# Kernel optimization log

Hardware: AMD Instinct MI355X
Metric: run time of the kernel (lower is better)

## Reference

```python
import jax, jax.numpy as jnp
import numpy as np

N = 100000   # nodes in batched graph
E = 1600000  # edges
B = 2048     # number of user/item pairs (target links)
IN = 4       # one-hot node label dim
H = 32       # latent dim per layer
R = 5        # num relations (rating levels)
NB = 2       # num bases
L = 4        # num conv layers


def setup_inputs() -> dict:
    key = jax.random.key(0)
    ks = jax.random.split(key, 16)
    s = 0.1
    # node labels: first B nodes are users (class 0), next B items (class 1), rest hop labels {2,3}
    cls = jax.random.randint(ks[0], (N,), 2, IN)
    cls = cls.at[:B].set(0).at[B:2 * B].set(1)
    x = jax.nn.one_hot(cls, IN, dtype=jnp.float32)
    src = jax.random.randint(ks[1], (E,), 0, N)
    dst = jax.random.randint(ks[2], (E,), 0, N)
    etype = jax.random.randint(ks[3], (E,), 0, R)
    V0 = jax.random.normal(ks[4], (NB, IN, H), jnp.float32) * s
    comp0 = jax.random.normal(ks[5], (R, NB), jnp.float32) * s
    loop0 = jax.random.normal(ks[6], (IN, H), jnp.float32) * s
    bias0 = jnp.zeros((H,), jnp.float32)
    Vs = jax.random.normal(ks[7], (L - 1, NB, H, H), jnp.float32) * s
    comps = jax.random.normal(ks[8], (L - 1, R, NB), jnp.float32) * s
    loops = jax.random.normal(ks[9], (L - 1, H, H), jnp.float32) * s
    biases = jnp.zeros((L - 1, H), jnp.float32)
    w1 = jax.random.normal(ks[10], (128, 2 * L * H), jnp.float32) * 0.05
    b1 = jnp.zeros((128,), jnp.float32)
    w2 = jax.random.normal(ks[11], (1, 128), jnp.float32) * 0.05
    b2 = jnp.zeros((1,), jnp.float32)
    return {"x": x, "src": src, "dst": dst, "etype": etype,
            "V0": V0, "comp0": comp0, "loop0": loop0, "bias0": bias0,
            "Vs": Vs, "comps": comps, "loops": loops, "biases": biases,
            "w1": w1, "b1": b1, "w2": w2, "b2": b2}


def _rgcn(h, src, dst, etype, V, comp, loopW, bias):
    # basis-decomposed RelGraphConv: W_r = sum_b comp[r,b] * V[b]
    # precompute per-basis transforms at nodes, then combine per edge by relation coeff
    xb = jnp.einsum('ni,bio->nbo', h, V)            # [N, NB, out]
    m = jnp.einsum('eb,ebo->eo', comp[etype], xb[src])  # [E, out]
    agg = jax.ops.segment_sum(m, dst, num_segments=h.shape[0])  # sum aggregation
    return agg + h @ loopW + bias                   # self-loop + bias


def reference(x, src, dst, etype, V0, comp0, loop0, bias0, Vs, comps, loops, biases, w1, b1, w2, b2):
    states = []
    h = jnp.tanh(_rgcn(x, src, dst, etype, V0, comp0, loop0, bias0))
    states.append(h)
    for i in range(L - 1):
        h = jnp.tanh(_rgcn(h, src, dst, etype, Vs[i], comps[i], loops[i], biases[i]))
        states.append(h)
    cs = jnp.concatenate(states, axis=1)            # [N, L*H]
    # users are nodes [0,B), items are nodes [B,2B) by construction (x[:,0]==1 / x[:,1]==1)
    feat = jnp.concatenate([cs[:B], cs[B:2 * B]], axis=1)  # [B, 2*L*H]
    hid = jax.nn.relu(feat @ w1.T + b1)             # dropout inactive (eval)
    out = (hid @ w2.T + b2)[:, 0] * 1               # multiply_by = 1
    return out
```

## Files before the change

### kernel.cpp

```cpp
#include <hip/hip_runtime.h>
#include <hip/hip_fp16.h>

constexpr int N_  = 100000;
constexpr int E_  = 1600000;
constexpr int B_  = 2048;
constexpr int NT_ = 2 * B_;

constexpr int NPB_SHIFT = 9;
constexpr int NPB = 1 << NPB_SHIFT;
constexpr int KB_ = (N_ + NPB - 1) / NPB;
constexpr int CAP_ = 9216;
constexpr int PCHUNK = 8192;
constexpr int NPBLK = (E_ + PCHUNK - 1) / PCHUNK;

__global__ __launch_bounds__(256) void init_kernel(
    const float* __restrict__ x, const float* __restrict__ w1,
    unsigned char* __restrict__ cls, int* __restrict__ flag,
    int* __restrict__ cnt, int* __restrict__ bcur, float* __restrict__ w1t)
{
    const int b = blockIdx.x, t = threadIdx.x;
    if (b < 391) {
        const int n = b * 256 + t;
        if (n < N_) {
            const float4 v = *(const float4*)(x + n * 4);
            cls[n] = v.y > 0.5f ? 1 : (v.z > 0.5f ? 2 : (v.w > 0.5f ? 3 : 0));
            flag[n] = 0;
        }
        if (b == 0 && t == 0) *cnt = 0;
    } else if (b < 519) {
        const int idx = (b - 391) * 256 + t;
        const int j = idx >> 8, k = idx & 255;
        w1t[k * 128 + j] = w1[idx];
    } else {
        if (t < KB_) bcur[t] = 0;
    }
}

__global__ __launch_bounds__(256) void partition_kernel(
    const int* __restrict__ src, const int* __restrict__ dst,
    const int* __restrict__ etype, int* __restrict__ bcur, int* __restrict__ ebuf)
{
    __shared__ int hist[KB_];
    __shared__ int gbase[KB_];
    __shared__ int lcur[KB_];
    const int t = threadIdx.x;
    for (int i = t; i < KB_; i += 256) { hist[i] = 0; lcur[i] = 0; }
    __syncthreads();
    const int e0 = blockIdx.x * PCHUNK;
    const int e1 = min(e0 + PCHUNK, E_);
    for (int i = e0 + t; i < e1; i += 256) atomicAdd(&hist[dst[i] >> NPB_SHIFT], 1);
    __syncthreads();
    for (int i = t; i < KB_; i += 256) if (hist[i]) gbase[i] = atomicAdd(&bcur[i], hist[i]);
    __syncthreads();
    for (int i = e0 + t; i < e1; i += 256) {
        const int d = dst[i];
        const int b = d >> NPB_SHIFT;
        const int lp = atomicAdd(&lcur[b], 1);
        ebuf[(size_t)b * CAP_ + gbase[b] + lp] = src[i] | (etype[i] << 17) | ((d & (NPB - 1)) << 20);
    }
}

__global__ __launch_bounds__(256) void bscan_kernel(
    const int* __restrict__ bcur, int* __restrict__ boffs)
{
    __shared__ int sh[256];
    const int t = threadIdx.x;
    const int v = (t < KB_) ? bcur[t] : 0;
    sh[t] = v; __syncthreads();
#pragma unroll
    for (int off = 1; off < 256; off <<= 1) {
        const int u = (t >= off) ? sh[t - off] : 0;
        __syncthreads();
        sh[t] += u;
        __syncthreads();
    }
    if (t < KB_) boffs[t] = sh[t] - v;
    if (t == 0) boffs[KB_] = E_;
}

__global__ __launch_bounds__(512) void bfinish_kernel(
    const int* __restrict__ bcur, const int* __restrict__ boffs,
    const int* __restrict__ ebuf, const unsigned char* __restrict__ cls,
    const float* __restrict__ comp0, const float* __restrict__ V0,
    const float* __restrict__ loop0, const float* __restrict__ bias0,
    int* __restrict__ rowptr, int* __restrict__ pack,
    float* __restrict__ cs, __half* __restrict__ hout)
{
    __shared__ int cnt[NPB];
    __shared__ int sh[NPB];
    __shared__ unsigned int hist[NPB * 20];
    __shared__ float sLoop[128], sV0[256], sBias[32], sCmp[10];
    const int b = blockIdx.x, t = threadIdx.x;
    const int s0 = b * CAP_;
    const int s1 = s0 + bcur[b];
    const int db = boffs[b];
    cnt[t] = 0;
    for (int i = t; i < NPB * 20; i += 512) hist[i] = 0u;
    if (t < 128) sLoop[t] = loop0[t];
    if (t < 256) sV0[t]   = V0[t];
    if (t < 32)  sBias[t] = bias0[t];
    if (t < 10)  sCmp[t]  = comp0[t];
    __syncthreads();
    for (int i = s0 + t; i < s1; i += 512) {
        const int p = ebuf[i];
        const int dloc = p >> 20;
        const int et = (p >> 17) & 7;
        const int c = cls[p & 0x1FFFF];
        atomicAdd(&cnt[dloc], 1);
        atomicAdd(&hist[dloc * 20 + et * 4 + c], 1u);
    }
    __syncthreads();
    const int v = cnt[t];
    sh[t] = v; __syncthreads();
#pragma unroll
    for (int off = 1; off < NPB; off <<= 1) {
        const int u = (t >= off) ? sh[t - off] : 0;
        __syncthreads();
        sh[t] += u;
        __syncthreads();
    }
    const int rp = db + sh[t] - v;
    const int node = (b << NPB_SHIFT) + t;
    if (node < N_) rowptr[node] = rp;
    cnt[t] = rp;
    if (b == 0 && t == 0) rowptr[N_] = E_;
    __syncthreads();
    for (int i = s0 + t; i < s1; i += 512) {
        const int p = ebuf[i];
        const int pos = atomicAdd(&cnt[p >> 20], 1);
        pack[pos] = p & 0xFFFFF;
    }
    if (node < N_) {
        float A0[4], A1[4];
#pragma unroll
        for (int j = 0; j < 4; ++j) {
            float a0 = 0.f, a1 = 0.f;
#pragma unroll
            for (int r = 0; r < 5; ++r) {
                const float c = (float)hist[t * 20 + r * 4 + j];
                a0 += c * sCmp[r * 2];
                a1 += c * sCmp[r * 2 + 1];
            }
            A0[j] = a0; A1[j] = a1;
        }
        const int myc = cls[node];
        __half hrow[32];
        const bool wcs = node < NT_;
#pragma unroll 8
        for (int d = 0; d < 32; ++d) {
            float o = sBias[d] + sLoop[myc * 32 + d];
#pragma unroll
            for (int j = 0; j < 4; ++j)
                o += A0[j] * sV0[j * 32 + d] + A1[j] * sV0[128 + j * 32 + d];
            const float r = tanhf(o);
            hrow[d] = __float2half(r);
            if (wcs) cs[node * 128 + d] = r;
        }
        uint4* dst4 = (uint4*)(hout + (size_t)node * 32);
        const uint4* src4 = (const uint4*)hrow;
        dst4[0] = src4[0]; dst4[1] = src4[1]; dst4[2] = src4[2]; dst4[3] = src4[3];
    }
}

__global__ __launch_bounds__(256) void flagcompact_kernel(
    const int* __restrict__ rowptr, const int* __restrict__ pack,
    int* __restrict__ flag, int* __restrict__ cnt, int* __restrict__ nlist)
{
    const int lim = rowptr[NT_];
    const int tid = blockIdx.x * 256 + threadIdx.x;
    if (tid < NT_) nlist[atomicAdd(cnt, 1)] = tid;
    const int stride = gridDim.x * 256;
    for (int i = tid; i < lim; i += stride) {
        const int s = pack[i] & 0x1FFFF;
        if (s >= NT_ && atomicExch(&flag[s], 1) == 0)
            nlist[atomicAdd(cnt, 1)] = s;
    }
}

__device__ __forceinline__ void acc_chunk(
    const uint4& v, int pq, bool ok, const float* cmp, float* a0, float* a1)
{
    const int tt = (pq >> 17) & 7;
    const float c0 = ok ? cmp[tt * 2]     : 0.f;
    const float c1 = ok ? cmp[tt * 2 + 1] : 0.f;
    const __half2* hp = (const __half2*)&v;
#pragma unroll
    for (int k = 0; k < 4; ++k) {
        const float2 f = __half22float2(hp[k]);
        a0[2 * k]     += c0 * f.x;
        a0[2 * k + 1] += c0 * f.y;
        a1[2 * k]     += c1 * f.x;
        a1[2 * k + 1] += c1 * f.y;
    }
}

__device__ __forceinline__ float gather_body(
    int n, int lane, int g,
    const __half* __restrict__ hin, const int* __restrict__ rowptr,
    const int* __restrict__ pack, const float* cmp,
    const float* __restrict__ V, const float* __restrict__ loopW,
    const float* __restrict__ bias, float (*hs)[96])
{
    hs[g][lane] = __half2float(hin[n * 32 + lane]);
    const int beg = rowptr[n], end = rowptr[n + 1];
    const int sg = lane >> 2;
    const int c  = lane & 31 & 3;
    const int i0 = beg + sg, i1 = i0 + 8, i2 = i0 + 16, i3 = i0 + 24;
    const int p0 = pack[i0 < end ? i0 : beg];
    const int p1 = pack[i1 < end ? i1 : beg];
    const int p2 = pack[i2 < end ? i2 : beg];
    const int p3 = pack[i3 < end ? i3 : beg];
    const uint4 v0 = *(const uint4*)(hin + (size_t)(p0 & 0x1FFFF) * 32 + c * 8);
    const uint4 v1 = *(const uint4*)(hin + (size_t)(p1 & 0x1FFFF) * 32 + c * 8);
    const uint4 v2 = *(const uint4*)(hin + (size_t)(p2 & 0x1FFFF) * 32 + c * 8);
    const uint4 v3 = *(const uint4*)(hin + (size_t)(p3 & 0x1FFFF) * 32 + c * 8);
    float a0[8] = {0.f,0.f,0.f,0.f,0.f,0.f,0.f,0.f};
    float a1[8] = {0.f,0.f,0.f,0.f,0.f,0.f,0.f,0.f};
    acc_chunk(v0, p0, i0 < end, cmp, a0, a1);
    acc_chunk(v1, p1, i1 < end, cmp, a0, a1);
    acc_chunk(v2, p2, i2 < end, cmp, a0, a1);
    acc_chunk(v3, p3, i3 < end, cmp, a0, a1);
    for (int e0 = beg + 32; e0 < end; e0 += 8) {
        const int e = e0 + sg;
        const bool ok = e < end;
        const int p = pack[ok ? e : beg];
        const uint4 u = *(const uint4*)(hin + (size_t)(p & 0x1FFFF) * 32 + c * 8);
        acc_chunk(u, p, ok, cmp, a0, a1);
    }
#pragma unroll
    for (int k = 0; k < 8; ++k) {
        a0[k] += __shfl_xor(a0[k], 4);
        a0[k] += __shfl_xor(a0[k], 8);
        a0[k] += __shfl_xor(a0[k], 16);
        a1[k] += __shfl_xor(a1[k], 4);
        a1[k] += __shfl_xor(a1[k], 8);
        a1[k] += __shfl_xor(a1[k], 16);
    }
    if (lane < 4) {
#pragma unroll
        for (int k = 0; k < 8; ++k) {
            hs[g][32 + c * 8 + k] = a0[k];
            hs[g][64 + c * 8 + k] = a1[k];
        }
    }
    __builtin_amdgcn_wave_barrier();
    float o = bias[lane];
#pragma unroll 8
    for (int k = 0; k < 32; ++k) {
        o += hs[g][k] * loopW[k * 32 + lane]
           + hs[g][32 + k] * V[k * 32 + lane]
           + hs[g][64 + k] * V[1024 + k * 32 + lane];
    }
    return tanhf(o);
}

__global__ __launch_bounds__(256) void gather_kernel(
    const __half* __restrict__ hin, const int* __restrict__ rowptr,
    const int* __restrict__ pack, const float* __restrict__ comp,
    const float* __restrict__ V, const float* __restrict__ loopW,
    const float* __restrict__ bias,
    float* __restrict__ cs, __half* __restrict__ hout, int out_off)
{
    __shared__ float hs[8][96];
    __shared__ float cmp[10];
    const int t = threadIdx.x, lane = t & 31, g = t >> 5;
    if (lane < 10) cmp[lane] = comp[lane];
    __builtin_amdgcn_wave_barrier();
    const int n = blockIdx.x * 8 + g;
    const float r = gather_body(n, lane, g, hin, rowptr, pack, cmp, V, loopW, bias, hs);
    if (n < NT_) cs[n * 128 + out_off + lane] = r;
    hout[n * 32 + lane] = __float2half(r);
}

__global__ __launch_bounds__(256) void gatherL_kernel(
    const __half* __restrict__ hin, const int* __restrict__ rowptr,
    const int* __restrict__ pack, const float* __restrict__ comp,
    const float* __restrict__ V, const float* __restrict__ loopW,
    const float* __restrict__ bias,
    const int* __restrict__ nlist, const int* __restrict__ cnt,
    float* __restrict__ cs, __half* __restrict__ hout, int out_off)
{
    __shared__ float hs[8][96];
    __shared__ float cmp[10];
    const int t = threadIdx.x, lane = t & 31, g = t >> 5;
    if (lane < 10) cmp[lane] = comp[lane];
    __builtin_amdgcn_wave_barrier();
    const int idx = blockIdx.x * 8 + g;
    if (idx >= *cnt) return;
    const int n = nlist[idx];
    const float r = gather_body(n, lane, g, hin, rowptr, pack, cmp, V, loopW, bias, hs);
    if (n < NT_) cs[n * 128 + out_off + lane] = r;
    hout[n * 32 + lane] = __float2half(r);
}

__global__ __launch_bounds__(128) void mlp_kernel(
    const __half* __restrict__ hin, const int* __restrict__ rowptr,
    const int* __restrict__ pack, const float* __restrict__ comp,
    const float* __restrict__ V, const float* __restrict__ loopW,
    const float* __restrict__ bias,
    const float* __restrict__ cs, const float* __restrict__ w1t,
    const float* __restrict__ b1, const float* __restrict__ w2,
    const float* __restrict__ b2, float* __restrict__ out)
{
    __shared__ float feat[256];
    __shared__ float hs[2][96];
    __shared__ float cmp[10];
    __shared__ float part[2];
    const int p = blockIdx.x, t = threadIdx.x;
    if (t < 10) cmp[t] = comp[t];
    if (t < 64) {
        const int g = t >> 5, lane = t & 31;
        const int n = g ? (B_ + p) : p;
        const float r = gather_body(n, lane, g, hin, rowptr, pack, cmp, V, loopW, bias, hs);
        feat[g * 128 + 96 + lane] = r;
    } else {
        const int i = t - 64;
        for (int j = i; j < 96; j += 64) {
            feat[j]       = cs[p * 128 + j];
            feat[128 + j] = cs[(B_ + p) * 128 + j];
        }
    }
    __syncthreads();
    float acc = b1[t];
#pragma unroll 8
    for (int k = 0; k < 256; ++k) acc += feat[k] * w1t[k * 128 + t];
    const float hid = acc > 0.f ? acc : 0.f;
    float v = w2[t] * hid;
#pragma unroll
    for (int off = 32; off > 0; off >>= 1) v += __shfl_down(v, off, 64);
    if ((t & 63) == 0) part[t >> 6] = v;
    __syncthreads();
    if (t == 0) out[p] = part[0] + part[1] + b2[0];
}

extern "C" void kernel_launch(void* const* d_in, const int* in_sizes, int n_in,
                              void* d_out, int out_size, void* d_ws, size_t ws_size,
                              hipStream_t stream) {
    const float* x      = (const float*)d_in[0];
    const int*   src    = (const int*)d_in[1];
    const int*   dst    = (const int*)d_in[2];
    const int*   etype  = (const int*)d_in[3];
    const float* V0     = (const float*)d_in[4];
    const float* comp0  = (const float*)d_in[5];
    const float* loop0  = (const float*)d_in[6];
    const float* bias0  = (const float*)d_in[7];
    const float* Vs     = (const float*)d_in[8];
    const float* comps  = (const float*)d_in[9];
    const float* loops  = (const float*)d_in[10];
    const float* biases = (const float*)d_in[11];
    const float* w1     = (const float*)d_in[12];
    const float* b1     = (const float*)d_in[13];
    const float* w2     = (const float*)d_in[14];
    const float* b2     = (const float*)d_in[15];
    float* out = (float*)d_out;

    float* ws   = (float*)d_ws;
    float* cs   = ws;
    float* w1t  = cs + (size_t)NT_ * 128;
    __half* hA  = (__half*)(w1t + 256 * 128);
    __half* hB  = hA + (size_t)N_ * 32;
    int* ebuf   = (int*)(hB + (size_t)N_ * 32);
    int* pack   = ebuf + (size_t)KB_ * CAP_;
    int* rowptr = pack + E_;
    int* flag   = rowptr + N_ + 1;
    int* cnt    = flag + N_;
    int* nlist  = cnt + 1;
    int* boffs  = nlist + N_;
    int* bcur   = boffs + KB_ + 1;
    unsigned char* cls = (unsigned char*)(bcur + KB_);

    const int gathBlocks = N_ / 8;

    init_kernel<<<520, 256, 0, stream>>>(x, w1, cls, flag, cnt, bcur, w1t);
    partition_kernel<<<NPBLK, 256, 0, stream>>>(src, dst, etype, bcur, ebuf);
    bscan_kernel<<<1, 256, 0, stream>>>(bcur, boffs);
    bfinish_kernel<<<KB_, 512, 0, stream>>>(bcur, boffs, ebuf, cls, comp0, V0, loop0, bias0,
                                            rowptr, pack, cs, hA);
    flagcompact_kernel<<<391, 256, 0, stream>>>(rowptr, pack, flag, cnt, nlist);
    gather_kernel<<<gathBlocks, 256, 0, stream>>>(
        hA, rowptr, pack, comps + 0, Vs + 0, loops + 0, biases + 0, cs, hB, 32);
    gatherL_kernel<<<gathBlocks, 256, 0, stream>>>(
        hB, rowptr, pack, comps + 10, Vs + 2048, loops + 1024, biases + 32,
        nlist, cnt, cs, hA, 64);
    mlp_kernel<<<B_, 128, 0, stream>>>(
        hA, rowptr, pack, comps + 20, Vs + 4096, loops + 2048, biases + 64,
        cs, w1t, b1, w2, b2, out);
}
```

Before: 187.2 us.

## Fuse bucket scan and frontier compaction into bfinish, accumulate gathers in half2

Removes the separate bucket-scan kernel by redoing the prefix scan inside every bfinish block. It moves frontier-node compaction into 8 extra bfinish blocks that read the partitioned edge buffer for the first dst buckets. Separately, it switches gather accumulation from fp32 FMAs to packed half2 FMAs with half-precision relation coefficients, which halves ALU work but adds fp16 rounding and overflow risk in the sums. Two launches are dropped in exchange for redundant per-block scans and reduced accumulation precision.

Measured after the change: 172.0 us. -8.1%, faster.

```diff
diff --git a/kernel.cpp b/kernel.cpp
--- a/kernel.cpp
+++ b/kernel.cpp
@@ -60,46 +60,54 @@
     }
 }
 
-__global__ __launch_bounds__(256) void bscan_kernel(
-    const int* __restrict__ bcur, int* __restrict__ boffs)
-{
-    __shared__ int sh[256];
-    const int t = threadIdx.x;
-    const int v = (t < KB_) ? bcur[t] : 0;
-    sh[t] = v; __syncthreads();
-#pragma unroll
-    for (int off = 1; off < 256; off <<= 1) {
-        const int u = (t >= off) ? sh[t - off] : 0;
-        __syncthreads();
-        sh[t] += u;
-        __syncthreads();
-    }
-    if (t < KB_) boffs[t] = sh[t] - v;
-    if (t == 0) boffs[KB_] = E_;
-}
-
 __global__ __launch_bounds__(512) void bfinish_kernel(
-    const int* __restrict__ bcur, const int* __restrict__ boffs,
-    const int* __restrict__ ebuf, const unsigned char* __restrict__ cls,
+    const int* __restrict__ bcur, const int* __restrict__ ebuf,
+    const unsigned char* __restrict__ cls,
     const float* __restrict__ comp0, const float* __restrict__ V0,
     const float* __restrict__ loop0, const float* __restrict__ bias0,
     int* __restrict__ rowptr, int* __restrict__ pack,
-    float* __restrict__ cs, __half* __restrict__ hout)
-{
+    float* __restrict__ cs, __half* __restrict__ hout,
+    int* __restrict__ flag, int* __restrict__ cnt_g, int* __restrict__ nlist)
+{
+    const int b = blockIdx.x, t = threadIdx.x;
+    if (b >= KB_) {
+        const int tb = b - KB_;
+        const int s0 = tb * CAP_;
+        const int s1 = s0 + bcur[tb];
+        const int nbase = tb << NPB_SHIFT;
+        for (int nn = nbase + t; nn < nbase + NPB; nn += 512)
+            nlist[atomicAdd(cnt_g, 1)] = nn;
+        for (int i = s0 + t; i < s1; i += 512) {
+            const int s = ebuf[i] & 0x1FFFF;
+            if (s >= NT_ && atomicExch(&flag[s], 1) == 0)
+                nlist[atomicAdd(cnt_g, 1)] = s;
+        }
+        return;
+    }
     __shared__ int cnt[NPB];
     __shared__ int sh[NPB];
     __shared__ unsigned int hist[NPB * 20];
     __shared__ float sLoop[128], sV0[256], sBias[32], sCmp[10];
-    const int b = blockIdx.x, t = threadIdx.x;
-    const int s0 = b * CAP_;
-    const int s1 = s0 + bcur[b];
-    const int db = boffs[b];
     cnt[t] = 0;
     for (int i = t; i < NPB * 20; i += 512) hist[i] = 0u;
     if (t < 128) sLoop[t] = loop0[t];
     if (t < 256) sV0[t]   = V0[t];
     if (t < 32)  sBias[t] = bias0[t];
     if (t < 10)  sCmp[t]  = comp0[t];
+    if (t < 256) sh[t] = (t < KB_) ? bcur[t] : 0;
+    __syncthreads();
+#pragma unroll
+    for (int off = 1; off < 256; off <<= 1) {
+        int u = 0;
+        if (t < 256 && t >= off) u = sh[t - off];
+        __syncthreads();
+        if (t < 256) sh[t] += u;
+        __syncthreads();
+    }
+    const int myCnt = bcur[b];
+    const int db = sh[b] - myCnt;
+    const int s0 = b * CAP_;
+    const int s1 = s0 + myCnt;
     __syncthreads();
     for (int i = s0 + t; i < s1; i += 512) {
         const int p = ebuf[i];
@@ -162,49 +170,33 @@
     }
 }
 
-__global__ __launch_bounds__(256) void flagcompact_kernel(
-    const int* __restrict__ rowptr, const int* __restrict__ pack,
-    int* __restrict__ flag, int* __restrict__ cnt, int* __restrict__ nlist)
-{
-    const int lim = rowptr[NT_];
-    const int tid = blockIdx.x * 256 + threadIdx.x;
-    if (tid < NT_) nlist[atomicAdd(cnt, 1)] = tid;
-    const int stride = gridDim.x * 256;
-    for (int i = tid; i < lim; i += stride) {
-        const int s = pack[i] & 0x1FFFF;
-        if (s >= NT_ && atomicExch(&flag[s], 1) == 0)
-            nlist[atomicAdd(cnt, 1)] = s;
-    }
-}
-
 __device__ __forceinline__ void acc_chunk(
-    const uint4& v, int pq, bool ok, const float* cmp, float* a0, float* a1)
+    const uint4& v, int pq, bool ok, const __half2* __restrict__ cmp2,
+    __half2* h0, __half2* h1)
 {
     const int tt = (pq >> 17) & 7;
-    const float c0 = ok ? cmp[tt * 2]     : 0.f;
-    const float c1 = ok ? cmp[tt * 2 + 1] : 0.f;
+    const __half2 z = __float2half2_rn(0.f);
+    const __half2 c0 = ok ? cmp2[tt * 2]     : z;
+    const __half2 c1 = ok ? cmp2[tt * 2 + 1] : z;
     const __half2* hp = (const __half2*)&v;
 #pragma unroll
     for (int k = 0; k < 4; ++k) {
-        const float2 f = __half22float2(hp[k]);
-        a0[2 * k]     += c0 * f.x;
-        a0[2 * k + 1] += c0 * f.y;
-        a1[2 * k]     += c1 * f.x;
-        a1[2 * k + 1] += c1 * f.y;
+        h0[k] = __hfma2(c0, hp[k], h0[k]);
+        h1[k] = __hfma2(c1, hp[k], h1[k]);
     }
 }
 
 __device__ __forceinline__ float gather_body(
     int n, int lane, int g,
     const __half* __restrict__ hin, const int* __restrict__ rowptr,
-    const int* __restrict__ pack, const float* cmp,
+    const int* __restrict__ pack, const __half2* __restrict__ cmp2,
     const float* __restrict__ V, const float* __restrict__ loopW,
     const float* __restrict__ bias, float (*hs)[96])
 {
     hs[g][lane] = __half2float(hin[n * 32 + lane]);
     const int beg = rowptr[n], end = rowptr[n + 1];
     const int sg = lane >> 2;
-    const int c  = lane & 31 & 3;
+    const int c  = lane & 3;
     const int i0 = beg + sg, i1 = i0 + 8, i2 = i0 + 16, i3 = i0 + 24;
     const int p0 = pack[i0 < end ? i0 : beg];
     const int p1 = pack[i1 < end ? i1 : beg];
@@ -214,18 +206,28 @@
     const uint4 v1 = *(const uint4*)(hin + (size_t)(p1 & 0x1FFFF) * 32 + c * 8);
     const uint4 v2 = *(const uint4*)(hin + (size_t)(p2 & 0x1FFFF) * 32 + c * 8);
     const uint4 v3 = *(const uint4*)(hin + (size_t)(p3 & 0x1FFFF) * 32 + c * 8);
-    float a0[8] = {0.f,0.f,0.f,0.f,0.f,0.f,0.f,0.f};
-    float a1[8] = {0.f,0.f,0.f,0.f,0.f,0.f,0.f,0.f};
-    acc_chunk(v0, p0, i0 < end, cmp, a0, a1);
-    acc_chunk(v1, p1, i1 < end, cmp, a0, a1);
-    acc_chunk(v2, p2, i2 < end, cmp, a0, a1);
-    acc_chunk(v3, p3, i3 < end, cmp, a0, a1);
+    __half2 h0[4], h1[4];
+    const __half2 z = __float2half2_rn(0.f);
+#pragma unroll
+    for (int k = 0; k < 4; ++k) { h0[k] = z; h1[k] = z; }
+    acc_chunk(v0, p0, i0 < end, cmp2, h0, h1);
+    acc_chunk(v1, p1, i1 < end, cmp2, h0, h1);
+    acc_chunk(v2, p2, i2 < end, cmp2, h0, h1);
+    acc_chunk(v3, p3, i3 < end, cmp2, h0, h1);
     for (int e0 = beg + 32; e0 < end; e0 += 8) {
         const int e = e0 + sg;
         const bool ok = e < end;
         const int p = pack[ok ? e : beg];
         const uint4 u = *(const uint4*)(hin + (size_t)(p & 0x1FFFF) * 32 + c * 8);
-        acc_chunk(u, p, ok, cmp, a0, a1);
+        acc_chunk(u, p, ok, cmp2, h0, h1);
+    }
+    float a0[8], a1[8];
+#pragma unroll
+    for (int k = 0; k < 4; ++k) {
+        const float2 f0 = __half22float2(h0[k]);
+        const float2 f1 = __half22float2(h1[k]);
+        a0[2 * k] = f0.x; a0[2 * k + 1] = f0.y;
+        a1[2 * k] = f1.x; a1[2 * k + 1] = f1.y;
     }
 #pragma unroll
     for (int k = 0; k < 8; ++k) {
@@ -262,12 +264,12 @@
     float* __restrict__ cs, __half* __restrict__ hout, int out_off)
 {
     __shared__ float hs[8][96];
-    __shared__ float cmp[10];
+    __shared__ __half2 cmp2[10];
     const int t = threadIdx.x, lane = t & 31, g = t >> 5;
-    if (lane < 10) cmp[lane] = comp[lane];
+    if (lane < 10) cmp2[lane] = __float2half2_rn(comp[lane]);
     __builtin_amdgcn_wave_barrier();
     const int n = blockIdx.x * 8 + g;
-    const float r = gather_body(n, lane, g, hin, rowptr, pack, cmp, V, loopW, bias, hs);
+    const float r = gather_body(n, lane, g, hin, rowptr, pack, cmp2, V, loopW, bias, hs);
     if (n < NT_) cs[n * 128 + out_off + lane] = r;
     hout[n * 32 + lane] = __float2half(r);
 }
@@ -281,14 +283,14 @@
     float* __restrict__ cs, __half* __restrict__ hout, int out_off)
 {
     __shared__ float hs[8][96];
-    __shared__ float cmp[10];
+    __shared__ __half2 cmp2[10];
     const int t = threadIdx.x, lane = t & 31, g = t >> 5;
-    if (lane < 10) cmp[lane] = comp[lane];
+    if (lane < 10) cmp2[lane] = __float2half2_rn(comp[lane]);
     __builtin_amdgcn_wave_barrier();
     const int idx = blockIdx.x * 8 + g;
     if (idx >= *cnt) return;
     const int n = nlist[idx];
-    const float r = gather_body(n, lane, g, hin, rowptr, pack, cmp, V, loopW, bias, hs);
+    const float r = gather_body(n, lane, g, hin, rowptr, pack, cmp2, V, loopW, bias, hs);
     if (n < NT_) cs[n * 128 + out_off + lane] = r;
     hout[n * 32 + lane] = __float2half(r);
 }
@@ -304,14 +306,14 @@
 {
     __shared__ float feat[256];
     __shared__ float hs[2][96];
-    __shared__ float cmp[10];
+    __shared__ __half2 cmp2[10];
     __shared__ float part[2];
     const int p = blockIdx.x, t = threadIdx.x;
-    if (t < 10) cmp[t] = comp[t];
+    if (t < 10) cmp2[t] = __float2half2_rn(comp[t]);
     if (t < 64) {
         const int g = t >> 5, lane = t & 31;
         const int n = g ? (B_ + p) : p;
-        const float r = gather_body(n, lane, g, hin, rowptr, pack, cmp, V, loopW, bias, hs);
+        const float r = gather_body(n, lane, g, hin, rowptr, pack, cmp2, V, loopW, bias, hs);
         feat[g * 128 + 96 + lane] = r;
     } else {
         const int i = t - 64;
@@ -365,18 +367,15 @@
     int* flag   = rowptr + N_ + 1;
     int* cnt    = flag + N_;
     int* nlist  = cnt + 1;
-    int* boffs  = nlist + N_;
-    int* bcur   = boffs + KB_ + 1;
+    int* bcur   = nlist + N_;
     unsigned char* cls = (unsigned char*)(bcur + KB_);
 
     const int gathBlocks = N_ / 8;
 
     init_kernel<<<520, 256, 0, stream>>>(x, w1, cls, flag, cnt, bcur, w1t);
     partition_kernel<<<NPBLK, 256, 0, stream>>>(src, dst, etype, bcur, ebuf);
-    bscan_kernel<<<1, 256, 0, stream>>>(bcur, boffs);
-    bfinish_kernel<<<KB_, 512, 0, stream>>>(bcur, boffs, ebuf, cls, comp0, V0, loop0, bias0,
-                                            rowptr, pack, cs, hA);
-    flagcompact_kernel<<<391, 256, 0, stream>>>(rowptr, pack, flag, cnt, nlist);
+    bfinish_kernel<<<KB_ + 8, 512, 0, stream>>>(bcur, ebuf, cls, comp0, V0, loop0, bias0,
+                                                rowptr, pack, cs, hA, flag, cnt, nlist);
     gather_kernel<<<gathBlocks, 256, 0, stream>>>(
         hA, rowptr, pack, comps + 0, Vs + 0, loops + 0, biases + 0, cs, hB, 32);
     gatherL_kernel<<<gathBlocks, 256, 0, stream>>>(
```
